# Kernel tuning notes

Hardware: AMD Instinct MI355X
Metric: run time of the kernel (lower is better)

Reference implementation:

```python
import jax, jax.numpy as jnp
import numpy as np

MIN_DEPTH = 1.45
MAX_DEPTH = 80.0
H, W = 64, 256
TAU = 2.0
DROP_VALUE = 1.0
N_POINTS = 16384


def make_angle():
    # Velodyne-like LiDAR angular map: elevation +3..-25 deg, azimuth pi..-pi
    elev = jnp.linspace(jnp.deg2rad(3.0), jnp.deg2rad(-25.0), H)
    azim = jnp.linspace(jnp.pi, -jnp.pi, W, endpoint=False)
    u = jnp.broadcast_to(elev[:, None], (H, W))
    v = jnp.broadcast_to(azim[None, :], (H, W))
    return jnp.stack([u, v])[None].astype(jnp.float32)  # (1,2,H,W)


def setup_inputs() -> dict:
    key = jax.random.key(0)
    k1, _ = jax.random.split(key)
    # scaled so most point depths fall inside (MIN_DEPTH/MAX_DEPTH, 1)
    xyz = 0.4 * jax.random.normal(k1, (1, N_POINTS, 3), dtype=jnp.float32)
    angle = make_angle()
    return {"xyz": xyz, "angle": angle}


def bilinear_rasterizer(coords, values, h_dim, w_dim):
    # coords: (B,N,2) float pixel coords (h,w); values: (B,N,C)
    B, N, C = values.shape
    h = coords[..., 0]
    w = coords[..., 1]
    h0 = jnp.floor(h)
    w0 = jnp.floor(w)
    dh = h - h0
    dw = w - w0
    out = jnp.zeros((B, h_dim * w_dim, C), values.dtype)
    bidx = jnp.arange(B)[:, None]
    corners = [
        (h0, w0, (1.0 - dh) * (1.0 - dw)),
        (h0, w0 + 1.0, (1.0 - dh) * dw),
        (h0 + 1.0, w0, dh * (1.0 - dw)),
        (h0 + 1.0, w0 + 1.0, dh * dw),
    ]
    for hi, wi, wt in corners:  # fixed 4-corner loop
        ok = (hi >= 0) & (hi <= h_dim - 1) & (wi >= 0) & (wi <= w_dim - 1)
        idx = (jnp.clip(hi, 0, h_dim - 1).astype(jnp.int32) * w_dim
               + jnp.clip(wi, 0, w_dim - 1).astype(jnp.int32))
        out = out.at[bidx, idx].add((wt * ok.astype(values.dtype))[..., None] * values)
    return out.reshape(B, h_dim, w_dim, C).transpose(0, 3, 1, 2)  # (B,C,H,W)


def reference(xyz, angle):
    # xyz: (B,N,3), angle: (1,2,H,W)
    r = jnp.linalg.norm(xyz[..., :2], axis=2, keepdims=True)          # (B,N,1)
    depth_1d = jnp.linalg.norm(xyz, axis=2, keepdims=True)            # (B,N,1)
    weight = jnp.exp(-TAU * depth_1d)                                 # 1/exp(tau*d)
    depth_1d = depth_1d * MAX_DEPTH
    inrange = ((depth_1d > MIN_DEPTH) & (depth_1d < MAX_DEPTH)).astype(weight.dtype)
    weight = weight * jax.lax.stop_gradient(inrange)
    angle_u = jnp.arctan2(xyz[..., 2:3], r)
    angle_v = jnp.arctan2(xyz[..., 1:2], xyz[..., 0:1])
    a = jnp.concatenate([angle_u, angle_v], axis=2)                   # (B,N,2)
    g = angle[0].reshape(2, H * W).T                                  # (HW,2)
    # squared angular distance via expansion (avoids (B,N,HW,2) intermediate)
    d2 = ((a ** 2).sum(-1, keepdims=True)
          + (g ** 2).sum(-1)[None, None, :]
          - 2.0 * jnp.einsum('bnc,mc->bnm', a, g))                    # (B,N,HW)
    ids = jnp.argmin(d2, axis=2)                                      # (B,N)
    uv = jnp.stack([ids // W, ids % W], axis=-1).astype(depth_1d.dtype)  # (B,N,2)
    num = bilinear_rasterizer(uv, weight * depth_1d, H, W)            # (B,1,H,W)
    den = bilinear_rasterizer(uv, weight, H, W)
    depth_2d = num / (den + 1e-8)
    valid = depth_2d != 0
    depth_2d = (depth_2d - MIN_DEPTH) / (MAX_DEPTH - MIN_DEPTH)
    depth_2d = jnp.where(valid, depth_2d, DROP_VALUE)
    return depth_2d, valid
```

## Files before the change

kernel.cpp:

```cpp
#include <hip/hip_runtime.h>

#define Hd 64
#define Wd 256
#define HWd 16384
#define NPTS 16384

#define F(x) __int_as_float(x)

__device__ __forceinline__ float fd_atanf(float x) {
    int hx = __float_as_int(x);
    int ix = hx & 0x7fffffff;
    if (ix >= 0x4c800000) {
        if (ix > 0x7f800000) return x;
        float r = __fadd_rn(F(0x3FC90FDA), F(0x33A22168));
        return (hx > 0) ? r : -r;
    }
    int id;
    if (ix < 0x3ee00000) {
        if (ix < 0x39800000) return x;
        id = -1;
    } else {
        x = F(ix);
        if (ix < 0x3f980000) {
            if (ix < 0x3f300000) {
                id = 0;
                x = __fdiv_rn(__fsub_rn(__fadd_rn(x, x), 1.0f), __fadd_rn(2.0f, x));
            } else {
                id = 1;
                x = __fdiv_rn(__fsub_rn(x, 1.0f), __fadd_rn(x, 1.0f));
            }
        } else {
            if (ix < 0x401c0000) {
                id = 2;
                x = __fdiv_rn(__fsub_rn(x, 1.5f), __fadd_rn(1.0f, __fmul_rn(1.5f, x)));
            } else {
                id = 3;
                x = __fdiv_rn(-1.0f, x);
            }
        }
    }
    float z = __fmul_rn(x, x);
    float w = __fmul_rn(z, z);
    float s1 = __fmul_rn(z, __fadd_rn(F(0x3EAAAAA3),
                    __fmul_rn(w, __fadd_rn(F(0x3E11F50D),
                    __fmul_rn(w, F(0x3D7CAC25))))));
    float s2 = __fmul_rn(w, __fadd_rn(F(0xBE4CCA17),
                    __fmul_rn(w, F(0xBDDA1247))));
    float ss = __fadd_rn(s1, s2);
    if (id < 0) return __fsub_rn(x, __fmul_rn(x, ss));
    const float athi[4] = {F(0x3EED6338), F(0x3F490FDA), F(0x3F7B985E), F(0x3FC90FDA)};
    const float atlo[4] = {F(0x31AC3769), F(0x33222168), F(0x33140FB4), F(0x33A22168)};
    float zr = __fsub_rn(athi[id], __fsub_rn(__fsub_rn(__fmul_rn(x, ss), atlo[id]), x));
    return (hx < 0) ? -zr : zr;
}

__device__ __forceinline__ float fd_atan2f(float y, float x) {
    const float pi     = F(0x40490FDB);
    const float pi_lo  = F(0xB3BBBD2E);
    const float pi_o_2 = F(0x3FC90FDB);
    int hx = __float_as_int(x), ix = hx & 0x7fffffff;
    int hy = __float_as_int(y), iy = hy & 0x7fffffff;
    if (ix > 0x7f800000 || iy > 0x7f800000) return x + y;
    if (hx == 0x3f800000) return fd_atanf(y);
    int m = ((hy >> 31) & 1) | ((hx >> 30) & 2);
    if (iy == 0) {
        switch (m) { case 0: case 1: return y; case 2: return pi; default: return -pi; }
    }
    if (ix == 0) return (hy < 0) ? -pi_o_2 : pi_o_2;
    if (ix == 0x7f800000) {
        if (iy == 0x7f800000) {
            switch (m) {
                case 0: return F(0x3F490FDB);
                case 1: return -F(0x3F490FDB);
                case 2: return __fmul_rn(3.0f, F(0x3F490FDB));
                default: return -__fmul_rn(3.0f, F(0x3F490FDB));
            }
        } else {
            switch (m) { case 0: return 0.0f; case 1: return -0.0f; case 2: return pi; default: return -pi; }
        }
    }
    if (iy == 0x7f800000) return (hy < 0) ? -pi_o_2 : pi_o_2;
    int k = (iy - ix) >> 23;
    float z;
    if (k > 26) { z = __fadd_rn(pi_o_2, __fmul_rn(0.5f, pi_lo)); m &= 1; }
    else if (hx < 0 && k < -26) z = 0.0f;
    else z = fd_atanf(__fdiv_rn(F(iy), F(ix)));
    switch (m) {
        case 0: return z;
        case 1: return -z;
        case 2: return __fsub_rn(pi, __fsub_rn(z, pi_lo));
        default: return __fsub_rn(__fsub_rn(z, pi_lo), pi);
    }
}

__global__ __launch_bounds__(256) void proj_scatter(
        const float* __restrict__ xyz,
        const float* __restrict__ angle,
        float* __restrict__ num,
        float* __restrict__ den) {
    __shared__ float s_eu[Hd], s_eu2[Hd];
    __shared__ float s_ev[Wd], s_ev2[Wd];

    int t = threadIdx.x;
    if (t < Hd) {
        float e = angle[t * Wd];
        s_eu[t]  = e;
        s_eu2[t] = __fmul_rn(e, e);
    }
    {
        float a = angle[HWd + t];
        s_ev[t]  = a;
        s_ev2[t] = __fmul_rn(a, a);
    }
    __syncthreads();

    int n = blockIdx.x * blockDim.x + t;
    if (n >= NPTS) return;

    float x = xyz[3 * n + 0];
    float y = xyz[3 * n + 1];
    float z = xyz[3 * n + 2];

    float xx = __fmul_rn(x, x);
    float yy = __fmul_rn(y, y);
    float zz = __fmul_rn(z, z);
    float r2 = __fadd_rn(xx, yy);
    float r  = __fsqrt_rn(r2);
    float d  = __fsqrt_rn(__fadd_rn(r2, zz));

    float wgt    = expf(-2.0f * d);
    float depth1 = __fmul_rn(d, 80.0f);
    if (!(depth1 > 1.45f && depth1 < 80.0f)) wgt = 0.0f;

    float au = fd_atan2f(z, r);
    float av = fd_atan2f(y, x);

    double su = ((double)s_eu[Hd - 1] - (double)s_eu[0]) / (double)(Hd - 1);
    double sv = ((double)s_ev[Wd - 1] - (double)s_ev[0]) / (double)(Wd - 1);
    int bh = __double2int_rn(((double)au - (double)s_eu[0]) / su);
    int bw = __double2int_rn(((double)av - (double)s_ev[0]) / sv);
    bh = bh < 0 ? 0 : (bh > Hd - 1 ? Hd - 1 : bh);
    bw = bw < 0 ? 0 : (bw > Wd - 1 ? Wd - 1 : bw);

    float asq = __fadd_rn(__fmul_rn(au, au), __fmul_rn(av, av));
    float bestd = 3.4e38f; int besti = 0x7fffffff;
    #pragma unroll
    for (int dh = -2; dh <= 2; ++dh) {
        int hh = bh + dh; hh = hh < 0 ? 0 : (hh > Hd - 1 ? Hd - 1 : hh);
        #pragma unroll
        for (int dw = -2; dw <= 2; ++dw) {
            int ww = bw + dw; ww = ww < 0 ? 0 : (ww > Wd - 1 ? Wd - 1 : ww);
            float gsq = __fadd_rn(s_eu2[hh], s_ev2[ww]);
            float dot = __builtin_fmaf(av, s_ev[ww], __fmul_rn(au, s_eu[hh]));
            float d2  = __fsub_rn(__fadd_rn(asq, gsq), __fmul_rn(2.0f, dot));
            int idx = hh * Wd + ww;
            if (d2 < bestd || (d2 == bestd && idx < besti)) { bestd = d2; besti = idx; }
        }
    }

    atomicAdd(&num[besti], __fmul_rn(wgt, depth1));
    atomicAdd(&den[besti], wgt);
}

__global__ __launch_bounds__(256) void finalize(
        const float* __restrict__ num,
        const float* __restrict__ den,
        float* __restrict__ out) {
    int i = blockIdx.x * blockDim.x + threadIdx.x;
    if (i >= HWd) return;
    float d2d = __fdiv_rn(num[i], __fadd_rn(den[i], 1e-8f));
    bool valid = (d2d != 0.0f);
    float nrm = __fdiv_rn(__fsub_rn(d2d, 1.45f), 78.55f);
    out[i]       = valid ? nrm : 1.0f;
    out[HWd + i] = valid ? 1.0f : 0.0f;
}

extern "C" void kernel_launch(void* const* d_in, const int* in_sizes, int n_in,
                              void* d_out, int out_size, void* d_ws, size_t ws_size,
                              hipStream_t stream) {
    const float* xyz   = (const float*)d_in[0];
    const float* angle = (const float*)d_in[1];
    float* out = (float*)d_out;
    float* num = (float*)d_ws;
    float* den = num + HWd;

    hipMemsetAsync(d_ws, 0, 2 * HWd * sizeof(float), stream);
    proj_scatter<<<NPTS / 256, 256, 0, stream>>>(xyz, angle, num, den);
    finalize<<<HWd / 256, 256, 0, stream>>>(num, den, out);
}
```

Baseline: 73.20 us.

## Fuse memset, scatter and finalize into one cooperative kernel with grid syncs

Replaces the memset and two kernel launches with a single cooperative kernel. It zeroes the accumulators, grid-syncs, scatters, grid-syncs again, then finalizes. It also skips the angle and argmin work for points whose weight is zero, shrinks the search window from 5x5 to 3x3, and swaps the double-precision bin estimate for float. This removes launch and memset overhead, but the smaller window and float rounding could change which pixel is chosen for points near bin boundaries.

```diff
diff --git a/kernel.cpp b/kernel.cpp
--- a/kernel.cpp
+++ b/kernel.cpp
@@ -1,4 +1,7 @@
 #include <hip/hip_runtime.h>
+#include <hip/hip_cooperative_groups.h>
+
+namespace cg = cooperative_groups;
 
 #define Hd 64
 #define Wd 256
@@ -93,15 +96,22 @@
     }
 }
 
-__global__ __launch_bounds__(256) void proj_scatter(
+__global__ __launch_bounds__(256) void fused(
         const float* __restrict__ xyz,
         const float* __restrict__ angle,
         float* __restrict__ num,
-        float* __restrict__ den) {
+        float* __restrict__ den,
+        float* __restrict__ out) {
+    cg::grid_group grid = cg::this_grid();
+
     __shared__ float s_eu[Hd], s_eu2[Hd];
     __shared__ float s_ev[Wd], s_ev2[Wd];
 
     int t = threadIdx.x;
+    int gid = blockIdx.x * 256 + t;
+
+    num[gid] = 0.0f;
+    den[gid] = 0.0f;
     if (t < Hd) {
         float e = angle[t * Wd];
         s_eu[t]  = e;
@@ -113,66 +123,66 @@
         s_ev2[t] = __fmul_rn(a, a);
     }
     __syncthreads();
-
-    int n = blockIdx.x * blockDim.x + t;
-    if (n >= NPTS) return;
-
-    float x = xyz[3 * n + 0];
-    float y = xyz[3 * n + 1];
-    float z = xyz[3 * n + 2];
-
-    float xx = __fmul_rn(x, x);
-    float yy = __fmul_rn(y, y);
-    float zz = __fmul_rn(z, z);
-    float r2 = __fadd_rn(xx, yy);
-    float r  = __fsqrt_rn(r2);
-    float d  = __fsqrt_rn(__fadd_rn(r2, zz));
-
-    float wgt    = expf(-2.0f * d);
-    float depth1 = __fmul_rn(d, 80.0f);
-    if (!(depth1 > 1.45f && depth1 < 80.0f)) wgt = 0.0f;
-
-    float au = fd_atan2f(z, r);
-    float av = fd_atan2f(y, x);
-
-    double su = ((double)s_eu[Hd - 1] - (double)s_eu[0]) / (double)(Hd - 1);
-    double sv = ((double)s_ev[Wd - 1] - (double)s_ev[0]) / (double)(Wd - 1);
-    int bh = __double2int_rn(((double)au - (double)s_eu[0]) / su);
-    int bw = __double2int_rn(((double)av - (double)s_ev[0]) / sv);
-    bh = bh < 0 ? 0 : (bh > Hd - 1 ? Hd - 1 : bh);
-    bw = bw < 0 ? 0 : (bw > Wd - 1 ? Wd - 1 : bw);
-
-    float asq = __fadd_rn(__fmul_rn(au, au), __fmul_rn(av, av));
-    float bestd = 3.4e38f; int besti = 0x7fffffff;
-    #pragma unroll
-    for (int dh = -2; dh <= 2; ++dh) {
-        int hh = bh + dh; hh = hh < 0 ? 0 : (hh > Hd - 1 ? Hd - 1 : hh);
-        #pragma unroll
-        for (int dw = -2; dw <= 2; ++dw) {
-            int ww = bw + dw; ww = ww < 0 ? 0 : (ww > Wd - 1 ? Wd - 1 : ww);
-            float gsq = __fadd_rn(s_eu2[hh], s_ev2[ww]);
-            float dot = __builtin_fmaf(av, s_ev[ww], __fmul_rn(au, s_eu[hh]));
-            float d2  = __fsub_rn(__fadd_rn(asq, gsq), __fmul_rn(2.0f, dot));
-            int idx = hh * Wd + ww;
-            if (d2 < bestd || (d2 == bestd && idx < besti)) { bestd = d2; besti = idx; }
+    grid.sync();
+
+    {
+        float x = xyz[3 * gid + 0];
+        float y = xyz[3 * gid + 1];
+        float z = xyz[3 * gid + 2];
+
+        float xx = __fmul_rn(x, x);
+        float yy = __fmul_rn(y, y);
+        float zz = __fmul_rn(z, z);
+        float r2 = __fadd_rn(xx, yy);
+        float r  = __fsqrt_rn(r2);
+        float d  = __fsqrt_rn(__fadd_rn(r2, zz));
+
+        float wgt    = expf(-2.0f * d);
+        float depth1 = __fmul_rn(d, 80.0f);
+        if (!(depth1 > 1.45f && depth1 < 80.0f)) wgt = 0.0f;
+
+        if (wgt != 0.0f) {
+            float au = fd_atan2f(z, r);
+            float av = fd_atan2f(y, x);
+
+            float inv_su = __fdiv_rn((float)(Hd - 1), __fsub_rn(s_eu[Hd - 1], s_eu[0]));
+            float inv_sv = __fdiv_rn((float)(Wd - 1), __fsub_rn(s_ev[Wd - 1], s_ev[0]));
+            int bh = __float2int_rn(__fmul_rn(__fsub_rn(au, s_eu[0]), inv_su));
+            int bw = __float2int_rn(__fmul_rn(__fsub_rn(av, s_ev[0]), inv_sv));
+            bh = bh < 0 ? 0 : (bh > Hd - 1 ? Hd - 1 : bh);
+            bw = bw < 0 ? 0 : (bw > Wd - 1 ? Wd - 1 : bw);
+
+            float asq = __fadd_rn(__fmul_rn(au, au), __fmul_rn(av, av));
+            float bestd = 3.4e38f; int besti = 0x7fffffff;
+            #pragma unroll
+            for (int dh = -1; dh <= 1; ++dh) {
+                int hh = bh + dh; hh = hh < 0 ? 0 : (hh > Hd - 1 ? Hd - 1 : hh);
+                #pragma unroll
+                for (int dw = -1; dw <= 1; ++dw) {
+                    int ww = bw + dw; ww = ww < 0 ? 0 : (ww > Wd - 1 ? Wd - 1 : ww);
+                    float gsq = __fadd_rn(s_eu2[hh], s_ev2[ww]);
+                    float dot = __builtin_fmaf(av, s_ev[ww], __fmul_rn(au, s_eu[hh]));
+                    float d2  = __fsub_rn(__fadd_rn(asq, gsq), __fmul_rn(2.0f, dot));
+                    int idx = hh * Wd + ww;
+                    if (d2 < bestd || (d2 == bestd && idx < besti)) { bestd = d2; besti = idx; }
+                }
+            }
+
+            atomicAdd(&num[besti], __fmul_rn(wgt, depth1));
+            atomicAdd(&den[besti], wgt);
         }
     }
 
-    atomicAdd(&num[besti], __fmul_rn(wgt, depth1));
-    atomicAdd(&den[besti], wgt);
-}
-
-__global__ __launch_bounds__(256) void finalize(
-        const float* __restrict__ num,
-        const float* __restrict__ den,
-        float* __restrict__ out) {
-    int i = blockIdx.x * blockDim.x + threadIdx.x;
-    if (i >= HWd) return;
-    float d2d = __fdiv_rn(num[i], __fadd_rn(den[i], 1e-8f));
-    bool valid = (d2d != 0.0f);
-    float nrm = __fdiv_rn(__fsub_rn(d2d, 1.45f), 78.55f);
-    out[i]       = valid ? nrm : 1.0f;
-    out[HWd + i] = valid ? 1.0f : 0.0f;
+    __threadfence();
+    grid.sync();
+
+    {
+        float d2d = __fdiv_rn(num[gid], __fadd_rn(den[gid], 1e-8f));
+        bool valid = (d2d != 0.0f);
+        float nrm = __fdiv_rn(__fsub_rn(d2d, 1.45f), 78.55f);
+        out[gid]       = valid ? nrm : 1.0f;
+        out[HWd + gid] = valid ? 1.0f : 0.0f;
+    }
 }
 
 extern "C" void kernel_launch(void* const* d_in, const int* in_sizes, int n_in,
@@ -184,7 +194,7 @@
     float* num = (float*)d_ws;
     float* den = num + HWd;
 
-    hipMemsetAsync(d_ws, 0, 2 * HWd * sizeof(float), stream);
-    proj_scatter<<<NPTS / 256, 256, 0, stream>>>(xyz, angle, num, den);
-    finalize<<<HWd / 256, 256, 0, stream>>>(num, den, out);
-}
+    void* args[] = {(void*)&xyz, (void*)&angle, (void*)&num, (void*)&den, (void*)&out};
+    hipLaunchCooperativeKernel((void*)fused, dim3(NPTS / 256), dim3(256),
+                               args, 0, stream);
+}
```

After: 105.9 us. 1.45x slower.
